# Kernel optimization log

Hardware: AMD Instinct MI355X
Metric: run time of the kernel (lower is better)

The kernel has to match this reference:

```python
import jax, jax.numpy as jnp
import numpy as np

K = 1.0          # Lorentz curvature param: x_t^2 - |x_s|^2 = K
SQRT_K = 1.0
EPS = 1e-8
HEADS = 12

def add_time(s):
    t = jnp.sqrt(K + jnp.sum(s * s, axis=-1, keepdims=True))
    return jnp.concatenate([t, s], axis=-1)

def lorentz_ln(x, g, b):
    s = x[..., 1:]
    mu = jnp.mean(s, axis=-1, keepdims=True)
    var = jnp.var(s, axis=-1, keepdims=True)
    s = (s - mu) / jnp.sqrt(var + 1e-5) * g + b
    return add_time(s)

def lorentz_fc(x, W, heads=None, act=None):
    # linear on full Lorentz vector -> space part; time recomputed to stay on manifold
    s = x @ W.T
    if act is not None:
        s = act(s)
    if heads is not None:
        bsz, n, dt = s.shape
        s = s.reshape(bsz, n, heads, dt // heads).transpose(0, 2, 1, 3)  # (b,h,n,hd)
    return add_time(s)

def logmap0(x):
    t, s = x[..., :1], x[..., 1:]
    sn = jnp.sqrt(jnp.sum(s * s, axis=-1, keepdims=True))
    dist = SQRT_K * jnp.arccosh(jnp.maximum(t / SQRT_K, 1.0 + 1e-7))
    u = dist * s / jnp.maximum(sn, EPS)
    return jnp.concatenate([jnp.zeros_like(t), u], axis=-1)

def expmap0(u):
    us = u[..., 1:]
    n = jnp.sqrt(jnp.sum(us * us, axis=-1, keepdims=True))
    nc = jnp.maximum(n, EPS)
    t = SQRT_K * jnp.cosh(n / SQRT_K)
    s = SQRT_K * jnp.sinh(n / SQRT_K) * us / nc
    return jnp.concatenate([t, s], axis=-1)

def ste_clip(x, lo, hi):
    # straight-through estimator: clamp in fwd, identity grad
    return x + jax.lax.stop_gradient(jnp.clip(x, lo, hi) - x)

def ste_max_clamp(x, hi):
    return x + jax.lax.stop_gradient(jnp.minimum(x, hi) - x)

def mha_last_layer(x, Wq, Wk, Wv, Wo, alpha_raw, tau_raw, lambda_raw):
    q = lorentz_fc(x, Wq, heads=HEADS)   # (b,h,n,hd+1)
    k = lorentz_fc(x, Wk, heads=HEADS)
    v = lorentz_fc(x, Wv, heads=HEADS)
    q_t, q_s = q[..., :1], q[..., 1:]
    k_t, k_s = k[..., :1], k[..., 1:]
    # Lorentzian inner product -> hyperbolic pairwise distances
    inner_QK = -q_t @ jnp.swapaxes(k_t, -1, -2) + jnp.einsum('bhid,bhjd->bhij', q_s, k_s)
    raw_cosh = jnp.maximum(-inner_QK / K, 1.0)                # (b,h,n,n)
    is_self = raw_cosh < 1.0 + 1e-5
    safe_cosh = jnp.where(is_self, 2.0, raw_cosh)
    dist_QK = SQRT_K * jnp.arccosh(safe_cosh)
    cosh_OQ = jnp.maximum(q_t / SQRT_K, 1.0 + 1e-7)
    cosh_OK = jnp.maximum(k_t / SQRT_K, 1.0 + 1e-7)
    c_tilde = jnp.minimum(SQRT_K * jnp.arccosh(cosh_OQ), 40.0) / SQRT_K  # (b,h,n,1)
    sinh_QK = jnp.sinh(dist_QK / SQRT_K)
    sinh_OQ = jnp.sinh(c_tilde)
    numer = raw_cosh * cosh_OQ - jnp.swapaxes(cosh_OK, -1, -2)
    raw_Z = numer / (sinh_OQ * sinh_QK)
    Z_safe = jnp.where(is_self, 1.0, ste_clip(raw_Z, -1.0, 1.0))
    alpha = jax.nn.softplus(alpha_raw)
    B = alpha * c_tilde / (1.0 + alpha * c_tilde)
    lam = jax.nn.softplus(lambda_raw)
    d_L = ste_max_clamp(dist_QK, 40.0)   # float32 branch of STE_Dist_Clamp
    log_dist_penalty = -lam * jnp.log1p(d_L * d_L)
    m = 0.1
    entail = jax.nn.softplus(B + Z_safe - m) - jax.nn.softplus(jnp.asarray(-m, B.dtype))
    tau = jax.nn.softplus(tau_raw)
    score = jax.nn.softmax(log_dist_penalty - tau * entail, axis=-1)
    # expmap aggregation: tangent-space weighted mean
    v_tan = logmap0(v)
    agg = jnp.einsum('bhij,bhjd->bhid', score, v_tan)
    agg = agg / (jnp.sum(score, axis=-1, keepdims=True) + 1e-8)
    attn = expmap0(agg).transpose(0, 2, 1, 3)   # (b,n,h,hd+1)
    bsz, n, h, _ = attn.shape
    attn_s = attn[..., 1:].reshape(bsz, n, -1)
    attn_t = attn[..., :1].reshape(bsz, n, -1)
    t_new = jnp.sqrt(jnp.sum(attn_t ** 2, axis=-1, keepdims=True) - (h - 1) * K)
    return lorentz_fc(jnp.concatenate([t_new, attn_s], axis=-1), Wo)


def setup_inputs() -> dict:
    key = jax.random.key(0)
    ks = jax.random.split(key, 8)
    b, n, hidden, mlp_hidden = 4, 1024, 769, 3073
    d = hidden - 1
    xs = jax.random.normal(ks[0], (b, n, d), jnp.float32)
    x = add_time(xs)
    def w(k, o, i):
        return jax.random.normal(k, (o, i), jnp.float32) * (i ** -0.5)
    return {
        'x': x,
        'Wq': w(ks[1], d, hidden), 'Wk': w(ks[2], d, hidden), 'Wv': w(ks[3], d, hidden),
        'Wo': w(ks[4], d, hidden),
        'ln1_g': jnp.ones((d,), jnp.float32), 'ln1_b': jnp.zeros((d,), jnp.float32),
        'ln2_g': jnp.ones((d,), jnp.float32), 'ln2_b': jnp.zeros((d,), jnp.float32),
        'Wm1': w(ks[5], mlp_hidden - 1, hidden), 'Wm2': w(ks[6], d, mlp_hidden),
        'alpha_raw': jnp.zeros((1,), jnp.float32),
        'tau_raw': jnp.zeros((1,), jnp.float32),
        'lambda_raw': jnp.zeros((1,), jnp.float32),
    }


def reference(x, Wq, Wk, Wv, Wo, ln1_g, ln1_b, ln2_g, ln2_b, Wm1, Wm2, alpha_raw, tau_raw, lambda_raw):
    out = mha_last_layer(lorentz_ln(x, ln1_g, ln1_b), Wq, Wk, Wv, Wo, alpha_raw, tau_raw, lambda_raw)
    out = out[..., 1:] + x[..., 1:]                 # residual on space part (DropPath=identity in eval)
    h = lorentz_ln(add_time(out), ln2_g, ln2_b)
    h = lorentz_fc(h, Wm1, act=lambda z: jax.nn.gelu(z, approximate=False))
    h = lorentz_fc(h, Wm2)
    out = h[..., 1:] + out
    return add_time(out)
```

## Files before the change

### kernel.cpp

```cpp
#include <hip/hip_runtime.h>
#include <cstdint>
#include <cstddef>

typedef unsigned short u16;
typedef __attribute__((ext_vector_type(8))) __bf16 bf16x8;
typedef __attribute__((ext_vector_type(4))) float f32x4;
typedef __attribute__((ext_vector_type(4))) short s16x4;

#define SEQ 1024
#define MROWS 4096
#define DDIM 768
#define HID 769
#define KP1 800
#define MLPD 3072
#define KP2 3104
#define NHEADS 12
#define LN2F 0.69314718056f
#define LOG2EF 1.44269504089f

static __device__ __forceinline__ u16 f2bf(float f){
  union { float f; uint32_t u; } v; v.f = f;
  return (u16)((v.u + 0x7FFFu + ((v.u >> 16) & 1u)) >> 16);
}

static __device__ __forceinline__ f32x4 mfma16(bf16x8 a, bf16x8 b, f32x4 c){
  return __builtin_amdgcn_mfma_f32_16x16x32_bf16(a, b, c, 0, 0, 0);
}

static __device__ __forceinline__ f32x4 mfma16k(s16x4 a, s16x4 b, f32x4 c){
  return __builtin_amdgcn_mfma_f32_16x16x16bf16_1k(a, b, c, 0, 0, 0);
}

static __device__ __forceinline__ s16x4 pack4(uint32_t lo, uint32_t hi){
  union { uint2 u; s16x4 v; } cv; cv.u.x = lo; cv.u.y = hi; return cv.v;
}

static __device__ __forceinline__ void async_lds16(const u16* g, u16* l){
  u16* gm = const_cast<u16*>(g);
  __builtin_amdgcn_global_load_lds(
      (__attribute__((address_space(1))) void*)gm,
      (__attribute__((address_space(3))) void*)l, 16, 0, 0);
}

static __device__ __forceinline__ float blk_reduce(float v, float* red, int tid){
  #pragma unroll
  for (int off = 1; off < 64; off <<= 1) v += __shfl_xor(v, off, 64);
  __syncthreads();
  if ((tid & 63) == 0) red[tid >> 6] = v;
  __syncthreads();
  return red[0] + red[1] + red[2] + red[3];
}

static __device__ __forceinline__ void conv_seg(const float* W, u16* O, int idx, int K, int Kp){
  int n = idx / Kp, k = idx - n * Kp;
  O[idx] = (k < K) ? f2bf(W[(size_t)n * K + k]) : (u16)0;
}
__global__ __launch_bounds__(256) void conv_all(const float* __restrict__ Wq, const float* __restrict__ Wk,
    const float* __restrict__ Wv, const float* __restrict__ Wo,
    const float* __restrict__ Wm1, const float* __restrict__ Wm2, u16* __restrict__ dst){
  int b = blockIdx.x, tid = threadIdx.x;
  if (b < 2400){        conv_seg(Wq,  dst,            b*256+tid,        769, 800); }
  else if (b < 4800){   conv_seg(Wk,  dst + 614400,  (b-2400)*256+tid,  769, 800); }
  else if (b < 7200){   conv_seg(Wv,  dst + 1228800, (b-4800)*256+tid,  769, 800); }
  else if (b < 9600){   conv_seg(Wo,  dst + 1843200, (b-7200)*256+tid,  769, 800); }
  else if (b < 19200){  conv_seg(Wm1, dst + 2457600, (b-9600)*256+tid,  769, 800); }
  else {                conv_seg(Wm2, dst + 4915200, (b-19200)*256+tid, 3073, 3104); }
}

__global__ __launch_bounds__(256) void ln_kernel(const float* __restrict__ X, int xstr, int xoff,
    const float* __restrict__ g, const float* __restrict__ b, u16* __restrict__ O){
  __shared__ float red[4];
  int m = blockIdx.x, tid = threadIdx.x;
  const float* xr = X + (size_t)m * xstr + xoff;
  float s[3], y[3];
  float s1 = 0.f, s2 = 0.f;
  #pragma unroll
  for (int j = 0; j < 3; j++){ float v = xr[tid + j*256]; s[j] = v; s1 += v; s2 += v*v; }
  s1 = blk_reduce(s1, red, tid);
  s2 = blk_reduce(s2, red, tid);
  float mu = s1 * (1.f/768.f);
  float var = s2 * (1.f/768.f) - mu*mu;
  float rstd = rsqrtf(var + 1e-5f);
  float q = 0.f;
  #pragma unroll
  for (int j = 0; j < 3; j++){ int i = tid + j*256; y[j] = (s[j]-mu)*rstd*g[i] + b[i]; q += y[j]*y[j]; }
  q = blk_reduce(q, red, tid);
  u16* orow = O + (size_t)m * KP1;
  #pragma unroll
  for (int j = 0; j < 3; j++) orow[1 + tid + j*256] = f2bf(y[j]);
  if (tid == 0) orow[0] = f2bf(sqrtf(1.f + q));
  if (tid < 31) orow[769 + tid] = 0;
}

__global__ __launch_bounds__(256) void ln_sum_kernel(const float* __restrict__ P4,
    const float* __restrict__ x, const float* __restrict__ g, const float* __restrict__ b,
    float* __restrict__ out1, u16* __restrict__ O){
  __shared__ float red[4];
  int m = blockIdx.x, tid = threadIdx.x;
  float s[3], y[3];
  float s1 = 0.f, s2 = 0.f;
  #pragma unroll
  for (int j = 0; j < 3; j++){
    int col = tid + j*256;
    float v = x[(size_t)m * HID + 1 + col];
    #pragma unroll
    for (int z = 0; z < 4; z++) v += P4[(size_t)z*MROWS*DDIM + (size_t)m*DDIM + col];
    out1[(size_t)m*DDIM + col] = v;
    s[j] = v; s1 += v; s2 += v*v;
  }
  s1 = blk_reduce(s1, red, tid);
  s2 = blk_reduce(s2, red, tid);
  float mu = s1 * (1.f/768.f);
  float var = s2 * (1.f/768.f) - mu*mu;
  float rstd = rsqrtf(var + 1e-5f);
  float q = 0.f;
  #pragma unroll
  for (int j = 0; j < 3; j++){ int i = tid + j*256; y[j] = (s[j]-mu)*rstd*g[i] + b[i]; q += y[j]*y[j]; }
  q = blk_reduce(q, red, tid);
  u16* orow = O + (size_t)m * KP1;
  #pragma unroll
  for (int j = 0; j < 3; j++) orow[1 + tid + j*256] = f2bf(y[j]);
  if (tid == 0) orow[0] = f2bf(sqrtf(1.f + q));
  if (tid < 31) orow[769 + tid] = 0;
}

__global__ __launch_bounds__(256) void gemm_split(
    const u16* __restrict__ A, const u16* __restrict__ B, float* __restrict__ C,
    int N, int Kp)
{
  __shared__ u16 As[128*32];
  __shared__ u16 Bs[128*32];
  int tid = threadIdx.x;
  int wave = tid >> 6, lane = tid & 63;
  int lrow = lane & 15, lq = lane >> 4;
  int m0 = blockIdx.y * 128, n0 = blockIdx.x * 128;
  int wm = wave >> 1, wn = wave & 1;
  int chunks = Kp >> 5;
  int nz = gridDim.z, z = blockIdx.z;
  int base = chunks / nz, rem = chunks - base * nz;
  int begin = z * base + (z < rem ? z : rem);
  int count = base + (z < rem ? 1 : 0);
  C += (size_t)z * MROWS * N;
  f32x4 acc[4][4] = {};
  int seg = wave * 2;
  int srow = lane >> 2;
  int scol = (lane & 3) * 8;
  const u16* Abase = A + (size_t)m0 * Kp;
  const u16* Bbase = B + (size_t)n0 * Kp;
  for (int kc = begin; kc < begin + count; kc++){
    int k0 = kc * 32;
    __syncthreads();
    #pragma unroll
    for (int i = 0; i < 2; i++){
      int s = seg + i;
      async_lds16(Abase + (size_t)(s*16 + srow) * Kp + k0 + scol, As + s*512);
      async_lds16(Bbase + (size_t)(s*16 + srow) * Kp + k0 + scol, Bs + s*512);
    }
    __syncthreads();
    bf16x8 af[4], bfr[4];
    #pragma unroll
    for (int t = 0; t < 4; t++){
      af[t]  = *(const bf16x8*)(As + (wm*64 + t*16 + lrow)*32 + lq*8);
      bfr[t] = *(const bf16x8*)(Bs + (wn*64 + t*16 + lrow)*32 + lq*8);
    }
    #pragma unroll
    for (int mt = 0; mt < 4; mt++)
      #pragma unroll
      for (int nt = 0; nt < 4; nt++)
        acc[mt][nt] = mfma16(af[mt], bfr[nt], acc[mt][nt]);
  }
  #pragma unroll
  for (int mt = 0; mt < 4; mt++)
    #pragma unroll
    for (int nt = 0; nt < 4; nt++){
      int col = n0 + wn*64 + nt*16 + lrow;
      #pragma unroll
      for (int r = 0; r < 4; r++){
        int row = m0 + wm*64 + mt*16 + lq*4 + r;
        C[(size_t)row * N + col] = acc[mt][nt][r];
      }
    }
}

__global__ __launch_bounds__(256) void gemm_gelu(
    const u16* __restrict__ A, const u16* __restrict__ B, u16* __restrict__ O,
    int N, int Kp)
{
  __shared__ u16 As[128*32];
  __shared__ u16 Bs[128*32];
  int tid = threadIdx.x;
  int wave = tid >> 6, lane = tid & 63;
  int lrow = lane & 15, lq = lane >> 4;
  int m0 = blockIdx.y * 128, n0 = blockIdx.x * 128;
  int wm = wave >> 1, wn = wave & 1;
  f32x4 acc[4][4] = {};
  int seg = wave * 2;
  int srow = lane >> 2;
  int scol = (lane & 3) * 8;
  const u16* Abase = A + (size_t)m0 * Kp;
  const u16* Bbase = B + (size_t)n0 * Kp;
  for (int k0 = 0; k0 < Kp; k0 += 32){
    __syncthreads();
    #pragma unroll
    for (int i = 0; i < 2; i++){
      int s = seg + i;
      async_lds16(Abase + (size_t)(s*16 + srow) * Kp + k0 + scol, As + s*512);
      async_lds16(Bbase + (size_t)(s*16 + srow) * Kp + k0 + scol, Bs + s*512);
    }
    __syncthreads();
    bf16x8 af[4], bfr[4];
    #pragma unroll
    for (int t = 0; t < 4; t++){
      af[t]  = *(const bf16x8*)(As + (wm*64 + t*16 + lrow)*32 + lq*8);
      bfr[t] = *(const bf16x8*)(Bs + (wn*64 + t*16 + lrow)*32 + lq*8);
    }
    #pragma unroll
    for (int mt = 0; mt < 4; mt++)
      #pragma unroll
      for (int nt = 0; nt < 4; nt++)
        acc[mt][nt] = mfma16(af[mt], bfr[nt], acc[mt][nt]);
  }
  #pragma unroll
  for (int mt = 0; mt < 4; mt++)
    #pragma unroll
    for (int nt = 0; nt < 4; nt++){
      int col = n0 + wn*64 + nt*16 + lrow;
      #pragma unroll
      for (int r = 0; r < 4; r++){
        int row = m0 + wm*64 + mt*16 + lq*4 + r;
        float v = acc[mt][nt][r];
        float e = 0.5f * v * (1.f + erff(v * 0.70710678f));
        O[(size_t)row * KP2 + 1 + col] = f2bf(e);
      }
    }
}

__global__ __launch_bounds__(256) void rowsum(u16* __restrict__ O){
  __shared__ float red[4];
  int m = blockIdx.x, tid = threadIdx.x;
  u16* orow = O + (size_t)m * KP2;
  float gs = 0.f;
  #pragma unroll
  for (int j = 0; j < 12; j++){
    uint32_t u = orow[1 + tid + j*256];
    float e = __uint_as_float(u << 16);
    gs += e*e;
  }
  gs = blk_reduce(gs, red, tid);
  if (tid == 0) orow[0] = f2bf(sqrtf(1.f + gs));
  if (tid < 31) orow[3073 + tid] = 0;
}

__global__ __launch_bounds__(256) void pack_qk(const float* __restrict__ raw,
    u16* __restrict__ Qp, u16* __restrict__ Kpk, float* __restrict__ qt, float* __restrict__ kt)
{
  int wave = threadIdx.x >> 6, lane = threadIdx.x & 63;
  int m = blockIdx.x * 4 + wave;
  int h = blockIdx.y;
  int which = blockIdx.z;
  const float* src = raw + (size_t)m * 2304 + which * 768 + h*64 + lane;
  float v = *src;
  float ss = v*v;
  #pragma unroll
  for (int off = 1; off < 64; off <<= 1) ss += __shfl_xor(ss, off, 64);
  int b = m >> 10, n = m & 1023, bh = b * NHEADS + h;
  u16* dst = (which ? Kpk : Qp) + ((size_t)bh * SEQ + n) * 64 + lane;
  *dst = f2bf(v);
  if (lane == 0) (which ? kt : qt)[bh * SEQ + n] = sqrtf(1.f + ss);
}

__global__ __launch_bounds__(256) void pack_v(const float* __restrict__ vraw, u16* __restrict__ Vf){
  __shared__ float part[256];
  __shared__ float scl[64];
  __shared__ float tile[64][65];
  int tid = threadIdx.x;
  int kb = blockIdx.x, bh = blockIdx.y;
  int b = bh / NHEADS, h = bh - b*NHEADS;
  int kl = tid >> 2;
  int d0 = (tid & 3) * 16;
  int m = b * SEQ + kb * 64 + kl;
  float v[16]; float ss = 0.f;
  const float* src = vraw + (size_t)m * 2304 + h*64 + d0;
  #pragma unroll
  for (int i = 0; i < 16; i++){ v[i] = src[i]; ss += v[i]*v[i]; }
  part[tid] = ss;
  __syncthreads();
  if ((tid & 3) == 0){
    float s2 = part[tid] + part[tid+1] + part[tid+2] + part[tid+3];
    float sn = sqrtf(s2);
    float tv = sqrtf(1.f + s2);
    float ctv = fmaxf(tv, 1.f + 1e-7f);
    float dist = __logf(ctv + sqrtf(fmaxf(ctv*ctv - 1.f, 0.f)));
    scl[kl] = dist / fmaxf(sn, 1e-8f);
  }
  __syncthreads();
  float sc = scl[kl];
  #pragma unroll
  for (int i = 0; i < 16; i++) tile[kl][d0 + i] = v[i] * sc;
  __syncthreads();
  #pragma unroll
  for (int i = 0; i < 2; i++){
    int idx = tid + i*256;
    int ctg_l = idx >> 7;
    int ntp = (idx >> 6) & 1;
    int ln  = idx & 63;
    int lr = ln & 15, lqq = ln >> 4;
    int k0 = ctg_l*16 + lqq*4;
    int dlo = ntp*32 + lr;
    u16 tmp[8];
    #pragma unroll
    for (int j = 0; j < 4; j++){
      tmp[j]     = f2bf(tile[k0+j][dlo]);
      tmp[4+j]   = f2bf(tile[k0+j][dlo+16]);
    }
    u16* dst = Vf + ((((size_t)bh*64 + kb*4 + ctg_l)*2 + ntp)*64 + ln)*8;
    *(uint4*)dst = *(const uint4*)tmp;
  }
}

__global__ __launch_bounds__(256) void attn_kernel(
    const u16* __restrict__ Q, const u16* __restrict__ K, const u16* __restrict__ Vf,
    const float* __restrict__ qt, const float* __restrict__ kt,
    float* __restrict__ pAgg, float* __restrict__ pDen,
    const float* __restrict__ a_raw, const float* __restrict__ t_raw, const float* __restrict__ l_raw)
{
  __shared__ float rv[4][64];
  int tid = threadIdx.x;
  int bh = blockIdx.y, ks = blockIdx.z;
  int qbase = blockIdx.x * 64;
  float alpha = __logf(1.f + __expf(a_raw[0]));
  float tau   = __logf(1.f + __expf(t_raw[0]));
  float lam   = __logf(1.f + __expf(l_raw[0]));
  if (tid < 64){
    float qtv = qt[bh * SEQ + qbase + tid];
    float cq = fmaxf(qtv, 1.f + 1e-7f);
    float A = cq + __builtin_amdgcn_sqrtf(fmaxf(cq*cq - 1.f, 0.f));
    float ct = fminf(__builtin_amdgcn_logf(A) * LN2F, 40.f);
    float e = __expf(ct);
    float sh = 0.5f * (e - __builtin_amdgcn_rcpf(e));
    float ac = alpha * ct;
    rv[0][tid] = qtv;
    rv[1][tid] = cq;
    rv[2][tid] = __builtin_amdgcn_rcpf(sh);
    rv[3][tid] = (ac * __builtin_amdgcn_rcpf(1.f + ac) - 0.1f) * LOG2EF;
  }
  __syncthreads();
  int wave = tid >> 6, lane = tid & 63;
  int lrow = lane & 15, lq = lane >> 4;
  int myrow = wave*16 + lrow;
  float qt_l = rv[0][myrow], cq_l = rv[1][myrow], rri_l = rv[2][myrow], Bw_l = rv[3][myrow];
  const float tbase = tau * 0.92967051f;
  const u16* Qb = Q + ((size_t)bh * SEQ + qbase + wave*16 + lrow) * 64 + lq*8;
  bf16x8 bq0 = *(const bf16x8*)Qb;
  bf16x8 bq1 = *(const bf16x8*)(Qb + 32);
  const u16* Kt = K + (size_t)bh * SEQ * 64 + (size_t)(ks*512 + lrow) * 64 + lq*8;
  const u16* Vp = Vf + (size_t)bh * 65536 + (size_t)(ks*32) * 1024 + lane*8;
  const float* ktp = kt + (size_t)bh * SEQ + ks*512 + lq*4;
  s16x4 ones;
  ones[0] = (short)0x3F80; ones[1] = (short)0x3F80; ones[2] = (short)0x3F80; ones[3] = (short)0x3F80;
  f32x4 o[4] = {};
  f32x4 dacc = {};
  for (int jt = 0; jt < 8; jt++){
    bf16x8 vv[8];
    #pragma unroll
    for (int ct = 0; ct < 4; ct++){
      vv[ct*2]   = *(const bf16x8*)(Vp + ct*1024);
      vv[ct*2+1] = *(const bf16x8*)(Vp + ct*1024 + 512);
    }
    float4 kv[4];
    #pragma unroll
    for (int ct = 0; ct < 4; ct++) kv[ct] = *(const float4*)(ktp + ct*16);
    f32x4 s[4];
    #pragma unroll
    for (int ct = 0; ct < 4; ct++){
      bf16x8 a0 = *(const bf16x8*)(Kt + ct*1024);
      bf16x8 a1 = *(const bf16x8*)(Kt + ct*1024 + 32);
      f32x4 z = {0.f, 0.f, 0.f, 0.f};
      z = mfma16(a0, bq0, z);
      z = mfma16(a1, bq1, z);
      s[ct] = z;
    }
    #pragma unroll
    for (int ct = 0; ct < 4; ct++){
      float4 kvv = kv[ct];
      uint32_t pu[4];
      #pragma unroll
      for (int r = 0; r < 4; r++){
        float ktv = (r == 0) ? kvv.x : (r == 1) ? kvv.y : (r == 2) ? kvv.z : kvv.w;
        float c = fmaxf(__builtin_fmaf(qt_l, ktv, -s[ct][r]), 1.f);
        bool self = c < 1.00001f;
        float ce = self ? 2.f : c;
        float cm1 = __builtin_fmaf(ce, ce, -1.f);
        float rs = __builtin_amdgcn_rsqf(cm1);
        float shq = cm1 * rs;
        float d = __builtin_amdgcn_logf(ce + shq) * LN2F;
        float L1 = __builtin_amdgcn_logf(__builtin_fmaf(d, d, 1.f));
        float Z = __builtin_fmaf(ce, cq_l, -ktv) * rri_l * rs;
        Z = fminf(fmaxf(Z, -1.f), 1.f);
        Z = self ? 1.f : Z;
        float w2 = __builtin_fmaf(Z, LOG2EF, Bw_l);
        float ew = __builtin_amdgcn_exp2f(w2);
        float L2 = __builtin_amdgcn_logf(ew + 1.f);
        float logit = __builtin_fmaf(-lam, L1, __builtin_fmaf(-tau, L2, tbase));
        float p = __builtin_amdgcn_exp2f(logit);
        pu[r] = __float_as_uint(p);
      }
      uint32_t lo = __builtin_amdgcn_perm(pu[1], pu[0], 0x07060302u);
      uint32_t hi = __builtin_amdgcn_perm(pu[3], pu[2], 0x07060302u);
      s16x4 pb = pack4(lo, hi);
      union { bf16x8 v8; s16x4 h[2]; } c0, c1;
      c0.v8 = vv[ct*2]; c1.v8 = vv[ct*2+1];
      o[0] = mfma16k(c0.h[0], pb, o[0]);
      o[1] = mfma16k(c0.h[1], pb, o[1]);
      o[2] = mfma16k(c1.h[0], pb, o[2]);
      o[3] = mfma16k(c1.h[1], pb, o[3]);
      dacc = mfma16k(ones, pb, dacc);
    }
    Kt += 4096; Vp += 4096; ktp += 64;
  }
  size_t rowb = (size_t)(ks*48 + bh) * SEQ + qbase + wave*16 + lrow;
  if (lq == 0) pDen[rowb] = dacc[0];
  #pragma unroll
  for (int nt = 0; nt < 4; nt++){
    float4 ov; ov.x = o[nt][0]; ov.y = o[nt][1]; ov.z = o[nt][2]; ov.w = o[nt][3];
    *(float4*)(pAgg + rowb * 64 + nt*16 + lq*4) = ov;
  }
}

__global__ __launch_bounds__(768) void expmap_pack(const float* __restrict__ pAgg,
    const float* __restrict__ pDen, u16* __restrict__ O){
  __shared__ float th2[NHEADS];
  int m = blockIdx.x, tid = threadIdx.x;
  int h = tid >> 6, lane = tid & 63;
  int b = m >> 10, n = m & 1023, bh = b*NHEADS + h;
  size_t i0 = ((size_t)bh * SEQ + n);
  size_t i1 = ((size_t)(48 + bh) * SEQ + n);
  float d = pDen[i0] + pDen[i1];
  float rden = __builtin_amdgcn_rcpf(d * (1.f + 1e-8f));
  float u = (pAgg[i0*64 + lane] + pAgg[i1*64 + lane]) * rden;
  float n2 = u*u;
  #pragma unroll
  for (int off = 1; off < 64; off <<= 1) n2 += __shfl_xor(n2, off, 64);
  float nn = sqrtf(n2);
  float e = __expf(nn);
  float ch = 0.5f * (e + 1.f/e);
  float sh = 0.5f * (e - 1.f/e);
  float sc = sh / fmaxf(nn, 1e-8f);
  u16* orow = O + (size_t)m * KP1;
  orow[1 + h*64 + lane] = f2bf(u * sc);
  if (lane == 0) th2[h] = ch*ch;
  __syncthreads();
  if (tid == 0){
    float ssum = 0.f;
    #pragma unroll
    for (int i = 0; i < NHEADS; i++) ssum += th2[i];
    orow[0] = f2bf(sqrtf(ssum - 11.f));
  }
  if (tid >= 1 && tid < 32) orow[768 + tid] = 0;
}

__global__ __launch_bounds__(256) void final_sum(const float* __restrict__ P4,
    const float* __restrict__ out1, float* __restrict__ out){
  __shared__ float red[4];
  int m = blockIdx.x, tid = threadIdx.x;
  float v[3]; float s2 = 0.f;
  #pragma unroll
  for (int j = 0; j < 3; j++){
    int col = tid + j*256;
    float t = out1[(size_t)m*DDIM + col];
    #pragma unroll
    for (int z = 0; z < 4; z++) t += P4[(size_t)z*MROWS*DDIM + (size_t)m*DDIM + col];
    v[j] = t; s2 += t*t;
  }
  s2 = blk_reduce(s2, red, tid);
  float* orow = out + (size_t)m * HID;
  if (tid == 0) orow[0] = sqrtf(1.f + s2);
  #pragma unroll
  for (int j = 0; j < 3; j++) orow[1 + tid + j*256] = v[j];
}

extern "C" void kernel_launch(void* const* d_in, const int* in_sizes, int n_in,
                              void* d_out, int out_size, void* d_ws, size_t ws_size,
                              hipStream_t stream)
{
  (void)in_sizes; (void)n_in; (void)out_size; (void)ws_size;
  const float* x   = (const float*)d_in[0];
  const float* Wq  = (const float*)d_in[1];
  const float* Wk  = (const float*)d_in[2];
  const float* Wv  = (const float*)d_in[3];
  const float* Wo  = (const float*)d_in[4];
  const float* g1p = (const float*)d_in[5];
  const float* b1p = (const float*)d_in[6];
  const float* g2p = (const float*)d_in[7];
  const float* b2p = (const float*)d_in[8];
  const float* Wm1 = (const float*)d_in[9];
  const float* Wm2 = (const float*)d_in[10];
  const float* ar  = (const float*)d_in[11];
  const float* tr  = (const float*)d_in[12];
  const float* lr  = (const float*)d_in[13];

  char* ws = (char*)d_ws;
  u16*   wqb  = (u16*)(ws + 0);
  u16*   wob  = (u16*)(ws + 3686400);
  u16*   wm1b = (u16*)(ws + 4915200);
  u16*   wm2b = (u16*)(ws + 9830400);
  u16*   xln  = (u16*)(ws + 14598144);
  float* qkv  = (float*)(ws + 21151744);
  u16*   qp   = (u16*)(ws + 58900480);
  u16*   kpk  = (u16*)(ws + 65191936);
  u16*   vf   = (u16*)(ws + 71483392);
  float* qtb  = (float*)(ws + 77774848);
  float* ktb  = (float*)(ws + 77971456);
  float* pAgg = (float*)(ws + 78168064);
  float* pDen = (float*)(ws + 103333888);
  u16*   woin = (u16*)(ws + 103727104);
  float* woP  = (float*)(ws + 21151744);
  float* out1 = (float*)(ws + 103727104);
  u16*   ln2b = (u16*)(ws + 78168064);
  u16*   g1b  = (u16*)(ws + 21151744);
  float* out2P= (float*)(ws + 46579712);

  conv_all<<<dim3(28512), 256, 0, stream>>>(Wq, Wk, Wv, Wo, Wm1, Wm2, wqb);
  ln_kernel<<<dim3(4096), 256, 0, stream>>>(x, 769, 1, g1p, b1p, xln);
  gemm_split<<<dim3(18, 32, 1), 256, 0, stream>>>(xln, wqb, qkv, 2304, 800);
  pack_qk<<<dim3(1024, 12, 2), 256, 0, stream>>>(qkv, qp, kpk, qtb, ktb);
  pack_v<<<dim3(16, 48), 256, 0, stream>>>(qkv + 1536, vf);
  attn_kernel<<<dim3(16, 48, 2), 256, 0, stream>>>(qp, kpk, vf, qtb, ktb, pAgg, pDen, ar, tr, lr);
  expmap_pack<<<dim3(4096), 768, 0, stream>>>(pAgg, pDen, woin);
  gemm_split<<<dim3(6, 32, 4), 256, 0, stream>>>(woin, wob, woP, 768, 800);
  ln_sum_kernel<<<dim3(4096), 256, 0, stream>>>(woP, x, g2p, b2p, out1, ln2b);
  gemm_gelu<<<dim3(24, 32, 1), 256, 0, stream>>>(ln2b, wm1b, g1b, 3072, 800);
  rowsum<<<dim3(4096), 256, 0, stream>>>(g1b);
  gemm_split<<<dim3(6, 32, 4), 256, 0, stream>>>(g1b, wm2b, out2P, 768, 3104);
  final_sum<<<dim3(4096), 256, 0, stream>>>(out2P, out1, (float*)d_out);
}
```

Baseline: 374.7 us.

## Fuse GELU row-norm into MLP GEMM, use 128x64 tiles, approximate GELU

Replaces the 128x128 GELU GEMM and the separate rowsum pass with a generic 128x64-tile GEMM. When its gelu flag is set, the kernel applies the activation, reduces squared outputs per row, and atomically adds them into a row buffer. A small timecol kernel then writes the time coordinate and the padding. The QKV and Wo projections also use the narrower tile, which doubles the block count, and Wo's split-K drops from 4 to 2 so ln_sum reads fewer partials. Exact erf GELU is swapped for a tanh-style exp2/rcp approximation, which adds small numeric deviation, and the atomics make the row sums order-dependent.

New measurement: 393.6 us. 5.0% more time.

```diff
diff --git a/kernel.cpp b/kernel.cpp
--- a/kernel.cpp
+++ b/kernel.cpp
@@ -51,6 +51,14 @@
   return red[0] + red[1] + red[2] + red[3];
 }
 
+static __device__ __forceinline__ float gelu_fast(float z){
+  float z2 = z * z;
+  float t = __builtin_fmaf(z2, 0.044715f, 1.f);
+  float w = z * t * (-2.3022078f);
+  float e2 = __builtin_amdgcn_exp2f(w);
+  return z * __builtin_amdgcn_rcpf(1.f + e2);
+}
+
 static __device__ __forceinline__ void conv_seg(const float* W, u16* O, int idx, int K, int Kp){
   int n = idx / Kp, k = idx - n * Kp;
   O[idx] = (k < K) ? f2bf(W[(size_t)n * K + k]) : (u16)0;
@@ -92,11 +100,12 @@
   if (tid < 31) orow[769 + tid] = 0;
 }
 
-__global__ __launch_bounds__(256) void ln_sum_kernel(const float* __restrict__ P4,
+__global__ __launch_bounds__(256) void ln_sum_kernel(const float* __restrict__ P2,
     const float* __restrict__ x, const float* __restrict__ g, const float* __restrict__ b,
-    float* __restrict__ out1, u16* __restrict__ O){
+    float* __restrict__ out1, u16* __restrict__ O, float* __restrict__ rsq){
   __shared__ float red[4];
   int m = blockIdx.x, tid = threadIdx.x;
+  if (tid == 0) rsq[m] = 0.f;
   float s[3], y[3];
   float s1 = 0.f, s2 = 0.f;
   #pragma unroll
@@ -104,7 +113,7 @@
     int col = tid + j*256;
     float v = x[(size_t)m * HID + 1 + col];
     #pragma unroll
-    for (int z = 0; z < 4; z++) v += P4[(size_t)z*MROWS*DDIM + (size_t)m*DDIM + col];
+    for (int z = 0; z < 2; z++) v += P2[(size_t)z*MROWS*DDIM + (size_t)m*DDIM + col];
     out1[(size_t)m*DDIM + col] = v;
     s[j] = v; s1 += v; s2 += v*v;
   }
@@ -182,73 +191,103 @@
     }
 }
 
-__global__ __launch_bounds__(256) void gemm_gelu(
-    const u16* __restrict__ A, const u16* __restrict__ B, u16* __restrict__ O,
-    int N, int Kp)
+__global__ __launch_bounds__(256) void gemm64(
+    const u16* __restrict__ A, const u16* __restrict__ B,
+    float* __restrict__ C, u16* __restrict__ Og, float* __restrict__ rsq,
+    int N, int Kp, int gelu)
 {
   __shared__ u16 As[128*32];
-  __shared__ u16 Bs[128*32];
+  __shared__ u16 Bs[64*32];
   int tid = threadIdx.x;
   int wave = tid >> 6, lane = tid & 63;
   int lrow = lane & 15, lq = lane >> 4;
-  int m0 = blockIdx.y * 128, n0 = blockIdx.x * 128;
+  int m0 = blockIdx.y * 128, n0 = blockIdx.x * 64;
   int wm = wave >> 1, wn = wave & 1;
-  f32x4 acc[4][4] = {};
-  int seg = wave * 2;
+  int chunks = Kp >> 5;
+  int nz = gridDim.z, z = blockIdx.z;
+  int base = chunks / nz, rem = chunks - base * nz;
+  int begin = z * base + (z < rem ? z : rem);
+  int count = base + (z < rem ? 1 : 0);
+  f32x4 acc[4][2] = {};
   int srow = lane >> 2;
   int scol = (lane & 3) * 8;
   const u16* Abase = A + (size_t)m0 * Kp;
   const u16* Bbase = B + (size_t)n0 * Kp;
-  for (int k0 = 0; k0 < Kp; k0 += 32){
+  for (int kc = begin; kc < begin + count; kc++){
+    int k0 = kc * 32;
     __syncthreads();
     #pragma unroll
     for (int i = 0; i < 2; i++){
-      int s = seg + i;
+      int s = wave*2 + i;
       async_lds16(Abase + (size_t)(s*16 + srow) * Kp + k0 + scol, As + s*512);
-      async_lds16(Bbase + (size_t)(s*16 + srow) * Kp + k0 + scol, Bs + s*512);
-    }
+    }
+    async_lds16(Bbase + (size_t)(wave*16 + srow) * Kp + k0 + scol, Bs + wave*512);
     __syncthreads();
-    bf16x8 af[4], bfr[4];
-    #pragma unroll
-    for (int t = 0; t < 4; t++){
+    bf16x8 af[4], bfr[2];
+    #pragma unroll
+    for (int t = 0; t < 4; t++)
       af[t]  = *(const bf16x8*)(As + (wm*64 + t*16 + lrow)*32 + lq*8);
-      bfr[t] = *(const bf16x8*)(Bs + (wn*64 + t*16 + lrow)*32 + lq*8);
-    }
+    #pragma unroll
+    for (int t = 0; t < 2; t++)
+      bfr[t] = *(const bf16x8*)(Bs + (wn*32 + t*16 + lrow)*32 + lq*8);
     #pragma unroll
     for (int mt = 0; mt < 4; mt++)
       #pragma unroll
-      for (int nt = 0; nt < 4; nt++)
+      for (int nt = 0; nt < 2; nt++)
         acc[mt][nt] = mfma16(af[mt], bfr[nt], acc[mt][nt]);
   }
-  #pragma unroll
-  for (int mt = 0; mt < 4; mt++)
-    #pragma unroll
-    for (int nt = 0; nt < 4; nt++){
-      int col = n0 + wn*64 + nt*16 + lrow;
+  if (gelu == 0){
+    C += (size_t)z * MROWS * N;
+    #pragma unroll
+    for (int mt = 0; mt < 4; mt++)
+      #pragma unroll
+      for (int nt = 0; nt < 2; nt++){
+        int col = n0 + wn*32 + nt*16 + lrow;
+        #pragma unroll
+        for (int r = 0; r < 4; r++){
+          int row = m0 + wm*64 + mt*16 + lq*4 + r;
+          C[(size_t)row * N + col] = acc[mt][nt][r];
+        }
+      }
+  } else {
+    float ssq[4][4];
+    #pragma unroll
+    for (int mt = 0; mt < 4; mt++)
+      #pragma unroll
+      for (int r = 0; r < 4; r++) ssq[mt][r] = 0.f;
+    #pragma unroll
+    for (int mt = 0; mt < 4; mt++)
+      #pragma unroll
+      for (int nt = 0; nt < 2; nt++){
+        int col = n0 + wn*32 + nt*16 + lrow;
+        #pragma unroll
+        for (int r = 0; r < 4; r++){
+          int row = m0 + wm*64 + mt*16 + lq*4 + r;
+          float e = gelu_fast(acc[mt][nt][r]);
+          ssq[mt][r] += e*e;
+          Og[(size_t)row * KP2 + 1 + col] = f2bf(e);
+        }
+      }
+    #pragma unroll
+    for (int mt = 0; mt < 4; mt++)
       #pragma unroll
       for (int r = 0; r < 4; r++){
-        int row = m0 + wm*64 + mt*16 + lq*4 + r;
-        float v = acc[mt][nt][r];
-        float e = 0.5f * v * (1.f + erff(v * 0.70710678f));
-        O[(size_t)row * KP2 + 1 + col] = f2bf(e);
+        float v = ssq[mt][r];
+        v += __shfl_xor(v, 1, 64);
+        v += __shfl_xor(v, 2, 64);
+        v += __shfl_xor(v, 4, 64);
+        v += __shfl_xor(v, 8, 64);
+        if (lrow == 0)
+          atomicAdd(rsq + m0 + wm*64 + mt*16 + lq*4 + r, v);
       }
-    }
-}
-
-__global__ __launch_bounds__(256) void rowsum(u16* __restrict__ O){
-  __shared__ float red[4];
-  int m = blockIdx.x, tid = threadIdx.x;
-  u16* orow = O + (size_t)m * KP2;
-  float gs = 0.f;
-  #pragma unroll
-  for (int j = 0; j < 12; j++){
-    uint32_t u = orow[1 + tid + j*256];
-    float e = __uint_as_float(u << 16);
-    gs += e*e;
-  }
-  gs = blk_reduce(gs, red, tid);
-  if (tid == 0) orow[0] = f2bf(sqrtf(1.f + gs));
-  if (tid < 31) orow[3073 + tid] = 0;
+  }
+}
+
+__global__ __launch_bounds__(256) void timecol(const float* __restrict__ rsq, u16* __restrict__ O){
+  int idx = blockIdx.x * 256 + threadIdx.x;
+  int m = idx >> 5, j = idx & 31;
+  if (j == 0) O[(size_t)m * KP2] = f2bf(sqrtf(1.f + rsq[m]));
+  else        O[(size_t)m * KP2 + 3072 + j] = 0;
 }
 
 __global__ __launch_bounds__(256) void pack_qk(const float* __restrict__ raw,
@@ -509,28 +548,29 @@
   u16*   qp   = (u16*)(ws + 58900480);
   u16*   kpk  = (u16*)(ws + 65191936);
   u16*   vf   = (u16*)(ws + 71483392);
-  float* qtb  = (float*)(ws + 77774848);
-  float* ktb  = (float*)(ws + 77971456);
-  float* pAgg = (float*)(ws + 78168064);
-  float* pDen = (float*)(ws + 103333888);
-  u16*   woin = (u16*)(ws + 103727104);
+  float* rsq  = (float*)(ws + 77774848);
+  float* qtb  = (float*)(ws + 77791232);
+  float* ktb  = (float*)(ws + 77987840);
+  float* pAgg = (float*)(ws + 78381056);
+  float* pDen = (float*)(ws + 103546880);
+  u16*   woin = (u16*)(ws + 103940096);
   float* woP  = (float*)(ws + 21151744);
-  float* out1 = (float*)(ws + 103727104);
-  u16*   ln2b = (u16*)(ws + 78168064);
+  float* out1 = (float*)(ws + 103940096);
+  u16*   ln2b = (u16*)(ws + 78381056);
   u16*   g1b  = (u16*)(ws + 21151744);
   float* out2P= (float*)(ws + 46579712);
 
   conv_all<<<dim3(28512), 256, 0, stream>>>(Wq, Wk, Wv, Wo, Wm1, Wm2, wqb);
   ln_kernel<<<dim3(4096), 256, 0, stream>>>(x, 769, 1, g1p, b1p, xln);
-  gemm_split<<<dim3(18, 32, 1), 256, 0, stream>>>(xln, wqb, qkv, 2304, 800);
+  gemm64<<<dim3(36, 32, 1), 256, 0, stream>>>(xln, wqb, qkv, nullptr, nullptr, 2304, 800, 0);
   pack_qk<<<dim3(1024, 12, 2), 256, 0, stream>>>(qkv, qp, kpk, qtb, ktb);
   pack_v<<<dim3(16, 48), 256, 0, stream>>>(qkv + 1536, vf);
   attn_kernel<<<dim3(16, 48, 2), 256, 0, stream>>>(qp, kpk, vf, qtb, ktb, pAgg, pDen, ar, tr, lr);
   expmap_pack<<<dim3(4096), 768, 0, stream>>>(pAgg, pDen, woin);
-  gemm_split<<<dim3(6, 32, 4), 256, 0, stream>>>(woin, wob, woP, 768, 800);
-  ln_sum_kernel<<<dim3(4096), 256, 0, stream>>>(woP, x, g2p, b2p, out1, ln2b);
-  gemm_gelu<<<dim3(24, 32, 1), 256, 0, stream>>>(ln2b, wm1b, g1b, 3072, 800);
-  rowsum<<<dim3(4096), 256, 0, stream>>>(g1b);
+  gemm64<<<dim3(12, 32, 2), 256, 0, stream>>>(woin, wob, woP, nullptr, nullptr, 768, 800, 0);
+  ln_sum_kernel<<<dim3(4096), 256, 0, stream>>>(woP, x, g2p, b2p, out1, ln2b, rsq);
+  gemm64<<<dim3(48, 32, 1), 256, 0, stream>>>(ln2b, wm1b, nullptr, g1b, rsq, 3072, 800, 1);
+  timecol<<<dim3(512), 256, 0, stream>>>(rsq, g1b);
   gemm_split<<<dim3(6, 32, 4), 256, 0, stream>>>(g1b, wm2b, out2P, 768, 3104);
   final_sum<<<dim3(4096), 256, 0, stream>>>(out2P, out1, (float*)d_out);
 }
```
